# Optimization experiments

Measured on AMD Instinct MI355X. Metric: run time of the kernel, lower is better.

## Reference

```python
import jax, jax.numpy as jnp
import numpy as np

N_EMBD = 1024  # C in forward; scale is C**-0.5 (full embed dim, per source)


def setup_inputs() -> dict:
    key = jax.random.key(0)
    k1, k2, k3, k4 = jax.random.split(key, 4)
    B, T, C, H = 4, 4096, N_EMBD, 64
    x = jax.random.normal(k1, (B, T, C), dtype=jnp.float32)
    # weights stored as [in, out] = [n_embd, head_size]
    Wq = jax.random.normal(k2, (C, H), dtype=jnp.float32) * (C ** -0.5)
    Wk = jax.random.normal(k3, (C, H), dtype=jnp.float32) * (C ** -0.5)
    Wv = jax.random.normal(k4, (C, H), dtype=jnp.float32) * (C ** -0.5)
    return {"x": x, "Wq": Wq, "Wk": Wk, "Wv": Wv}


def reference(x, Wq, Wk, Wv):
    # x: [B, T, C]; projections to head_size H
    C = x.shape[-1]
    q = jnp.einsum('btc,ch->bth', x, Wq)  # [B,T,H]
    k = jnp.einsum('btc,ch->bth', x, Wk)  # [B,T,H]
    v = jnp.einsum('btc,ch->bth', x, Wv)  # [B,T,H]
    # scores scaled by C**-0.5 (full embed dim, matching original module)
    wei = jnp.einsum('bth,bsh->bts', q, k) * (C ** -0.5)  # [B,T,T]
    wei = jax.nn.softmax(wei, axis=-1)  # dropout p=0 -> identity
    out = jnp.einsum('bts,bsh->bth', wei, v)  # [B,T,H]
    return out
```

## Files before the change

### kernel.cpp

```cpp
#include <hip/hip_runtime.h>
#include <hip/hip_bf16.h>


#define BB 4
#define TT 4096
#define CC 1024
#define HH 64

typedef __attribute__((ext_vector_type(8))) short bf16x8;
typedef __attribute__((ext_vector_type(4))) float f32x4;

__device__ __forceinline__ short f2bf(float f) {
  union { float f; unsigned u; } v; v.f = f;
  unsigned r = v.u + 0x7fffu + ((v.u >> 16) & 1u);
  return (short)(r >> 16);
}

__global__ void wtf_kernel(const float* __restrict__ Wq, const float* __restrict__ Wk,
                           const float* __restrict__ Wv, short* __restrict__ WtF) {
  int idx = blockIdx.x * 256 + threadIdx.x;
  int lane = idx & 63, ks = (idx >> 6) & 31, nf = idx >> 11;
  int l15 = lane & 15, lg = lane >> 4;
  int n = nf * 16 + l15;
  const float* W = (n < HH) ? Wq : ((n < 2 * HH) ? Wk : Wv);
  float sc = (n < HH) ? (0.03125f * 1.44269504f) : 1.0f;
  int k0 = ks * 32 + lg * 8, h = n & (HH - 1);
  bf16x8 r;
#pragma unroll
  for (int j = 0; j < 8; ++j) r[j] = f2bf(W[(k0 + j) * HH + h] * sc);
  *(bf16x8*)(WtF + (size_t)idx * 8) = r;
}

__launch_bounds__(256, 4)
__global__ void proj_kernel(const float* __restrict__ x, const short* __restrict__ WtF,
                            short* __restrict__ qo, short* __restrict__ ko,
                            short* __restrict__ vTo) {
  __shared__ __align__(16) short xs[16 * 1024];
  int t = threadIdx.x;
  int row0 = blockIdx.x * 16;

  {
    int r = t >> 4, kc = t & 15;
    const float4* xr4 = (const float4*)(x + (size_t)(row0 + r) * CC) + kc * 2;
#pragma unroll
    for (int i = 0; i < 8; ++i) {
      float4 a = xr4[i * 32], b2 = xr4[i * 32 + 1];
      bf16x8 w;
      w[0] = f2bf(a.x);  w[1] = f2bf(a.y);  w[2] = f2bf(a.z);  w[3] = f2bf(a.w);
      w[4] = f2bf(b2.x); w[5] = f2bf(b2.y); w[6] = f2bf(b2.z); w[7] = f2bf(b2.w);
      int c = kc + i * 16;
      int S = (c * 256 + r * 16) ^ ((c & 7) << 4);
      *(bf16x8*)((char*)xs + S) = w;
    }
  }
  __syncthreads();

  int wave = t >> 6, lane = t & 63;
  int l15 = lane & 15, lg = lane >> 4;
  int nf0 = wave * 3;
  const short* wp = WtF + ((size_t)nf0 * 32 * 64 + (size_t)lane) * 8;
  const char* xsb = (const char*)xs;

  f32x4 acc[3];
#pragma unroll
  for (int j = 0; j < 3; ++j) acc[j] = (f32x4){0.f, 0.f, 0.f, 0.f};

  bf16x8 wA[3], wB[3];
#pragma unroll
  for (int j = 0; j < 3; ++j) wA[j] = *(const bf16x8*)(wp + (size_t)j * 32 * 512);

#pragma unroll
  for (int ks = 0; ks < 32; ks += 2) {
#pragma unroll
    for (int j = 0; j < 3; ++j)
      wB[j] = *(const bf16x8*)(wp + ((size_t)j * 32 + ks + 1) * 512);
    bf16x8 a0 = *(const bf16x8*)(xsb + ks * 1024 +
                   ((lane * 16) ^ ((((ks * 4) + lg) & 7) << 4)));
#pragma unroll
    for (int j = 0; j < 3; ++j)
      acc[j] = __builtin_amdgcn_mfma_f32_16x16x32_bf16(a0, wA[j], acc[j], 0, 0, 0);
    if (ks + 2 < 32) {
#pragma unroll
      for (int j = 0; j < 3; ++j)
        wA[j] = *(const bf16x8*)(wp + ((size_t)j * 32 + ks + 2) * 512);
    }
    bf16x8 a1 = *(const bf16x8*)(xsb + (ks + 1) * 1024 +
                   ((lane * 16) ^ (((((ks + 1) * 4) + lg) & 7) << 4)));
#pragma unroll
    for (int j = 0; j < 3; ++j)
      acc[j] = __builtin_amdgcn_mfma_f32_16x16x32_bf16(a1, wB[j], acc[j], 0, 0, 0);
  }

#pragma unroll
  for (int j = 0; j < 3; ++j) {
    int nf = nf0 + j;
    int h = (nf & 3) * 16 + l15;
    if (nf < 8) {
      short* dst = (nf < 4) ? qo : ko;
#pragma unroll
      for (int reg = 0; reg < 4; ++reg)
        dst[(size_t)(row0 + lg * 4 + reg) * HH + h] = f2bf(acc[j][reg]);
    } else {
      int b = row0 >> 12;
      int trow = (row0 & 4095) + lg * 4;
      short4 s4;
      s4.x = f2bf(acc[j][0]); s4.y = f2bf(acc[j][1]);
      s4.z = f2bf(acc[j][2]); s4.w = f2bf(acc[j][3]);
      *(short4*)(vTo + ((size_t)b * HH + h) * TT + trow) = s4;
    }
  }
}

__global__ void kperm_kernel(const short* __restrict__ k, short* __restrict__ kF) {
  int idx = blockIdx.x * 256 + threadIdx.x;
  int lane = idx & 63, ld = (idx >> 6) & 7, kt = (idx >> 9) & 63, b = idx >> 15;
  int l15 = lane & 15, lg = lane >> 4;
  int kpos = kt * 64 + (ld >> 1) * 16 + l15;
  int e0 = (ld & 1) * 32 + lg * 8;
  bf16x8 r = *(const bf16x8*)(k + ((size_t)b * TT + kpos) * HH + e0);
  *(bf16x8*)(kF + (size_t)idx * 8) = r;
}

__global__ void vperm_kernel(const short* __restrict__ vT, short* __restrict__ vF) {
  int idx = blockIdx.x * 256 + threadIdx.x;
  int lane = idx & 63, ld = (idx >> 6) & 7, kt = (idx >> 9) & 63, b = idx >> 15;
  int l15 = lane & 15, lg = lane >> 4;
  int h = (ld >> 1) * 16 + l15;
  int spos = kt * 64 + (ld & 1) * 32 + lg * 8;
  bf16x8 r = *(const bf16x8*)(vT + ((size_t)b * HH + h) * TT + spos);
  *(bf16x8*)(vF + (size_t)idx * 8) = r;
}

__launch_bounds__(512, 2)
__global__ void attnQ_kernel(const short* __restrict__ q, const short* __restrict__ kF,
                             const short* __restrict__ vF, float* __restrict__ out) {
  __shared__ __align__(16) short ps[8][1280];
  __shared__ __align__(16) float macc[64][68];
  __shared__ float lL[64];
  int wave = threadIdx.x >> 6, lane = threadIdx.x & 63;
  int l15 = lane & 15, lg = lane >> 4;
  int qg = wave & 1, qr = wave >> 1;
  int low3 = blockIdx.x & 7;
  int b  = low3 >> 1;
  int qt = ((blockIdx.x >> 3) << 1) | (low3 & 1);
  int brow0 = qt * 64;
  int rowW = brow0 + qg * 32;

  const short* qb = q + ((size_t)b * TT + rowW + l15) * HH;
  bf16x8 qa[2][2];
  qa[0][0] = *(const bf16x8*)(qb + lg * 8);
  qa[0][1] = *(const bf16x8*)(qb + 32 + lg * 8);
  qa[1][0] = *(const bf16x8*)(qb + 16 * HH + lg * 8);
  qa[1][1] = *(const bf16x8*)(qb + 16 * HH + 32 + lg * 8);

  const short* kfb = kF + (size_t)b * (64 * 8 * 64 * 8) + (size_t)lane * 8;
  const short* vfb = vF + (size_t)b * (64 * 8 * 64 * 8) + (size_t)lane * 8;

  f32x4 acc[2][4];
#pragma unroll
  for (int g = 0; g < 2; ++g)
#pragma unroll
    for (int i = 0; i < 4; ++i) acc[g][i] = (f32x4){0.f, 0.f, 0.f, 0.f};
  float lsum[2][4] = {{0.f, 0.f, 0.f, 0.f}, {0.f, 0.f, 0.f, 0.f}};

  char* psw = (char*)&ps[wave][0];
  int pw = lg * 4 * 80 + ((l15 * 2) ^ ((lg >> 1) << 4));
  int pr = l15 * 80 + ((lg ^ (l15 >> 3)) << 4);

  for (int t = qr * 32; t < qr * 32 + 32; ++t) {
    const short* kp = kfb + (size_t)t * 2048;
    const short* vp = vfb + (size_t)(t >> 1) * 4096 + (size_t)(t & 1) * 512;
    bf16x8 kf[4], vf[4];
#pragma unroll
    for (int ld = 0; ld < 4; ++ld) kf[ld] = *(const bf16x8*)(kp + ld * 512);
#pragma unroll
    for (int hf = 0; hf < 4; ++hf) vf[hf] = *(const bf16x8*)(vp + hf * 1024);
#pragma unroll
    for (int g = 0; g < 2; ++g)
#pragma unroll
      for (int cf = 0; cf < 2; ++cf) {
        f32x4 t4 = (f32x4){0.f, 0.f, 0.f, 0.f};
        t4 = __builtin_amdgcn_mfma_f32_16x16x32_bf16(qa[g][0], kf[cf * 2], t4, 0, 0, 0);
        t4 = __builtin_amdgcn_mfma_f32_16x16x32_bf16(qa[g][1], kf[cf * 2 + 1], t4, 0, 0, 0);
#pragma unroll
        for (int reg = 0; reg < 4; ++reg) {
          float p = exp2f(t4[reg]);
          lsum[g][reg] += p;
          *(short*)(psw + (g * 1280 + pw + reg * 80 + cf * 32)) = f2bf(p);
        }
      }
    bf16x8 pa0 = *(const bf16x8*)(psw + pr);
    bf16x8 pa1 = *(const bf16x8*)(psw + 1280 + pr);
    __builtin_amdgcn_s_setprio(1);
#pragma unroll
    for (int hf = 0; hf < 4; ++hf) {
      acc[0][hf] = __builtin_amdgcn_mfma_f32_16x16x32_bf16(pa0, vf[hf], acc[0][hf], 0, 0, 0);
      acc[1][hf] = __builtin_amdgcn_mfma_f32_16x16x32_bf16(pa1, vf[hf], acc[1][hf], 0, 0, 0);
    }
    __builtin_amdgcn_s_setprio(0);
  }

#pragma unroll
  for (int g = 0; g < 2; ++g)
#pragma unroll
    for (int reg = 0; reg < 4; ++reg) {
      float r = lsum[g][reg];
      r += __shfl_xor(r, 1); r += __shfl_xor(r, 2);
      r += __shfl_xor(r, 4); r += __shfl_xor(r, 8);
      lsum[g][reg] = r;
    }

#pragma unroll
  for (int ph = 0; ph < 4; ++ph) {
    if (qr == ph) {
#pragma unroll
      for (int g = 0; g < 2; ++g) {
#pragma unroll
        for (int reg = 0; reg < 4; ++reg) {
          int row = qg * 32 + g * 16 + lg * 4 + reg;
          if (ph == 0) {
#pragma unroll
            for (int hf = 0; hf < 4; ++hf)
              macc[row][hf * 16 + l15] = acc[g][hf][reg];
            if (l15 == 0) lL[row] = lsum[g][reg];
          } else {
#pragma unroll
            for (int hf = 0; hf < 4; ++hf)
              macc[row][hf * 16 + l15] += acc[g][hf][reg];
            if (l15 == 0) lL[row] += lsum[g][reg];
          }
        }
      }
    }
    __syncthreads();
  }

  {
    int t = threadIdx.x;
    int r = t >> 3, c0 = (t & 7) * 8;
    float linv = 1.0f / lL[r];
    float4 o0, o1;
    o0.x = macc[r][c0 + 0] * linv; o0.y = macc[r][c0 + 1] * linv;
    o0.z = macc[r][c0 + 2] * linv; o0.w = macc[r][c0 + 3] * linv;
    o1.x = macc[r][c0 + 4] * linv; o1.y = macc[r][c0 + 5] * linv;
    o1.z = macc[r][c0 + 6] * linv; o1.w = macc[r][c0 + 7] * linv;
    float* op = out + ((size_t)b * TT + brow0 + r) * HH + c0;
    *(float4*)op = o0;
    *(float4*)(op + 4) = o1;
  }
}

extern "C" void kernel_launch(void* const* d_in, const int* in_sizes, int n_in,
                              void* d_out, int out_size, void* d_ws, size_t ws_size,
                              hipStream_t stream) {
  const float* x  = (const float*)d_in[0];
  const float* Wq = (const float*)d_in[1];
  const float* Wk = (const float*)d_in[2];
  const float* Wv = (const float*)d_in[3];
  float* out = (float*)d_out;

  char* ws = (char*)d_ws;
  short* WtF = (short*)ws;
  short* q   = (short*)(ws + 0x080000);
  short* k   = (short*)(ws + 0x280000);
  short* vT  = (short*)(ws + 0x480000);
  short* kF  = (short*)(ws + 0x680000);
  short* vF  = (short*)(ws + 0x880000);

  hipLaunchKernelGGL(wtf_kernel,   dim3(96),   dim3(256), 0, stream, Wq, Wk, Wv, WtF);
  hipLaunchKernelGGL(proj_kernel,  dim3(1024), dim3(256), 0, stream, x, WtF, q, k, vT);
  hipLaunchKernelGGL(kperm_kernel, dim3(512),  dim3(256), 0, stream, k, kF);
  hipLaunchKernelGGL(vperm_kernel, dim3(512),  dim3(256), 0, stream, vT, vF);
  hipLaunchKernelGGL(attnQ_kernel, dim3(256),  dim3(512), 0, stream, q, kF, vF, out);
}
```

Baseline: 76.28 us.

## Give each attention wave all 64 query rows and double-buffer K/V register loads

The attention kernel now splits the key range across all 8 waves, each wave covering all 64 query rows (4 row groups) instead of 32 rows over 4 key splits. Each loaded K/V fragment is therefore reused across twice as many query rows, which cuts global/L2 traffic per MFMA. The next key tile is prefetched into a second register set while the current one is computed, to hide load latency. Probabilities are converted with the library bf16 conversion. The cost is more registers (larger accumulators plus double buffers), more LDS for P, and an 8-phase reduction of partial results.

```diff
diff --git a/kernel.cpp b/kernel.cpp
--- a/kernel.cpp
+++ b/kernel.cpp
@@ -14,6 +14,11 @@
   union { float f; unsigned u; } v; v.f = f;
   unsigned r = v.u + 0x7fffu + ((v.u >> 16) & 1u);
   return (short)(r >> 16);
+}
+
+__device__ __forceinline__ short f2bf_hw(float f) {
+  __hip_bfloat16 h = __float2bfloat16(f);
+  return *reinterpret_cast<short*>(&h);
 }
 
 __global__ void wtf_kernel(const float* __restrict__ Wq, const float* __restrict__ Wk,
@@ -131,77 +136,101 @@
   *(bf16x8*)(vF + (size_t)idx * 8) = r;
 }
 
-__launch_bounds__(512, 2)
-__global__ void attnQ_kernel(const short* __restrict__ q, const short* __restrict__ kF,
-                             const short* __restrict__ vF, float* __restrict__ out) {
-  __shared__ __align__(16) short ps[8][1280];
+
+#define A64_BODY(KC, VC, KN, VN, T_CUR)                                         \
+  {                                                                             \
+    int tn_ = ((T_CUR) + 1 < ktN) ? (T_CUR) + 1 : kt0;                          \
+    const short* kpn_ = kfb + (size_t)tn_ * 2048;                               \
+    const short* vpn_ = vfb + (size_t)(tn_ >> 1) * 4096 + (size_t)(tn_ & 1) * 512; \
+    _Pragma("unroll")                                                           \
+    for (int ld = 0; ld < 4; ++ld) KN[ld] = *(const bf16x8*)(kpn_ + ld * 512);  \
+    _Pragma("unroll")                                                           \
+    for (int hf = 0; hf < 4; ++hf) VN[hf] = *(const bf16x8*)(vpn_ + hf * 1024); \
+    _Pragma("unroll")                                                           \
+    for (int g = 0; g < 4; ++g) {                                               \
+      _Pragma("unroll")                                                         \
+      for (int cf = 0; cf < 2; ++cf) {                                          \
+        f32x4 t4_ = (f32x4){0.f, 0.f, 0.f, 0.f};                                \
+        t4_ = __builtin_amdgcn_mfma_f32_16x16x32_bf16(qa[g][0], KC[cf * 2], t4_, 0, 0, 0); \
+        t4_ = __builtin_amdgcn_mfma_f32_16x16x32_bf16(qa[g][1], KC[cf * 2 + 1], t4_, 0, 0, 0); \
+        _Pragma("unroll")                                                       \
+        for (int reg = 0; reg < 4; ++reg) {                                     \
+          float p_ = exp2f(t4_[reg]);                                           \
+          lsum[g][reg] += p_;                                                   \
+          *(short*)(psw + (g * 1280 + pw + reg * 80 + cf * 32)) = f2bf_hw(p_);  \
+        }                                                                       \
+      }                                                                         \
+    }                                                                           \
+    __builtin_amdgcn_s_setprio(1);                                              \
+    _Pragma("unroll")                                                           \
+    for (int g = 0; g < 4; ++g) {                                               \
+      bf16x8 pa_ = *(const bf16x8*)(psw + g * 1280 + pr);                       \
+      _Pragma("unroll")                                                         \
+      for (int hf = 0; hf < 4; ++hf)                                            \
+        acc[g][hf] = __builtin_amdgcn_mfma_f32_16x16x32_bf16(pa_, VC[hf], acc[g][hf], 0, 0, 0); \
+    }                                                                           \
+    __builtin_amdgcn_s_setprio(0);                                              \
+  }
+
+__global__ __launch_bounds__(512) __attribute__((amdgpu_waves_per_eu(2, 2)))
+void attn64_kernel(const short* __restrict__ q, const short* __restrict__ kF,
+                   const short* __restrict__ vF, float* __restrict__ out) {
+  __shared__ __align__(16) short ps[8][2560];
   __shared__ __align__(16) float macc[64][68];
   __shared__ float lL[64];
   int wave = threadIdx.x >> 6, lane = threadIdx.x & 63;
   int l15 = lane & 15, lg = lane >> 4;
-  int qg = wave & 1, qr = wave >> 1;
+  int qr = wave;
   int low3 = blockIdx.x & 7;
   int b  = low3 >> 1;
   int qt = ((blockIdx.x >> 3) << 1) | (low3 & 1);
   int brow0 = qt * 64;
-  int rowW = brow0 + qg * 32;
-
-  const short* qb = q + ((size_t)b * TT + rowW + l15) * HH;
-  bf16x8 qa[2][2];
-  qa[0][0] = *(const bf16x8*)(qb + lg * 8);
-  qa[0][1] = *(const bf16x8*)(qb + 32 + lg * 8);
-  qa[1][0] = *(const bf16x8*)(qb + 16 * HH + lg * 8);
-  qa[1][1] = *(const bf16x8*)(qb + 16 * HH + 32 + lg * 8);
+
+  const short* qb = q + ((size_t)b * TT + brow0 + l15) * HH;
+  bf16x8 qa[4][2];
+#pragma unroll
+  for (int g = 0; g < 4; ++g) {
+    qa[g][0] = *(const bf16x8*)(qb + g * 16 * HH + lg * 8);
+    qa[g][1] = *(const bf16x8*)(qb + g * 16 * HH + 32 + lg * 8);
+  }
 
   const short* kfb = kF + (size_t)b * (64 * 8 * 64 * 8) + (size_t)lane * 8;
   const short* vfb = vF + (size_t)b * (64 * 8 * 64 * 8) + (size_t)lane * 8;
 
-  f32x4 acc[2][4];
-#pragma unroll
-  for (int g = 0; g < 2; ++g)
+  f32x4 acc[4][4];
+#pragma unroll
+  for (int g = 0; g < 4; ++g)
 #pragma unroll
     for (int i = 0; i < 4; ++i) acc[g][i] = (f32x4){0.f, 0.f, 0.f, 0.f};
-  float lsum[2][4] = {{0.f, 0.f, 0.f, 0.f}, {0.f, 0.f, 0.f, 0.f}};
+  float lsum[4][4];
+#pragma unroll
+  for (int g = 0; g < 4; ++g)
+#pragma unroll
+    for (int i = 0; i < 4; ++i) lsum[g][i] = 0.f;
 
   char* psw = (char*)&ps[wave][0];
-  int pw = lg * 4 * 80 + ((l15 * 2) ^ ((lg >> 1) << 4));
+  int pw = lg * 320 + ((l15 * 2) ^ ((lg >> 1) << 4));
   int pr = l15 * 80 + ((lg ^ (l15 >> 3)) << 4);
 
-  for (int t = qr * 32; t < qr * 32 + 32; ++t) {
-    const short* kp = kfb + (size_t)t * 2048;
-    const short* vp = vfb + (size_t)(t >> 1) * 4096 + (size_t)(t & 1) * 512;
-    bf16x8 kf[4], vf[4];
-#pragma unroll
-    for (int ld = 0; ld < 4; ++ld) kf[ld] = *(const bf16x8*)(kp + ld * 512);
-#pragma unroll
-    for (int hf = 0; hf < 4; ++hf) vf[hf] = *(const bf16x8*)(vp + hf * 1024);
-#pragma unroll
-    for (int g = 0; g < 2; ++g)
-#pragma unroll
-      for (int cf = 0; cf < 2; ++cf) {
-        f32x4 t4 = (f32x4){0.f, 0.f, 0.f, 0.f};
-        t4 = __builtin_amdgcn_mfma_f32_16x16x32_bf16(qa[g][0], kf[cf * 2], t4, 0, 0, 0);
-        t4 = __builtin_amdgcn_mfma_f32_16x16x32_bf16(qa[g][1], kf[cf * 2 + 1], t4, 0, 0, 0);
-#pragma unroll
-        for (int reg = 0; reg < 4; ++reg) {
-          float p = exp2f(t4[reg]);
-          lsum[g][reg] += p;
-          *(short*)(psw + (g * 1280 + pw + reg * 80 + cf * 32)) = f2bf(p);
-        }
-      }
-    bf16x8 pa0 = *(const bf16x8*)(psw + pr);
-    bf16x8 pa1 = *(const bf16x8*)(psw + 1280 + pr);
-    __builtin_amdgcn_s_setprio(1);
-#pragma unroll
-    for (int hf = 0; hf < 4; ++hf) {
-      acc[0][hf] = __builtin_amdgcn_mfma_f32_16x16x32_bf16(pa0, vf[hf], acc[0][hf], 0, 0, 0);
-      acc[1][hf] = __builtin_amdgcn_mfma_f32_16x16x32_bf16(pa1, vf[hf], acc[1][hf], 0, 0, 0);
-    }
-    __builtin_amdgcn_s_setprio(0);
-  }
-
-#pragma unroll
-  for (int g = 0; g < 2; ++g)
+  int kt0 = qr * 16, ktN = kt0 + 16;
+
+  bf16x8 kcA[4], vcA[4], kcB[4], vcB[4];
+  {
+    const short* kp = kfb + (size_t)kt0 * 2048;
+    const short* vp = vfb + (size_t)(kt0 >> 1) * 4096 + (size_t)(kt0 & 1) * 512;
+#pragma unroll
+    for (int ld = 0; ld < 4; ++ld) kcA[ld] = *(const bf16x8*)(kp + ld * 512);
+#pragma unroll
+    for (int hf = 0; hf < 4; ++hf) vcA[hf] = *(const bf16x8*)(vp + hf * 1024);
+  }
+
+  for (int t = kt0; t < ktN; t += 2) {
+    A64_BODY(kcA, vcA, kcB, vcB, t)
+    A64_BODY(kcB, vcB, kcA, vcA, t + 1)
+  }
+
+#pragma unroll
+  for (int g = 0; g < 4; ++g)
 #pragma unroll
     for (int reg = 0; reg < 4; ++reg) {
       float r = lsum[g][reg];
@@ -211,13 +240,13 @@
     }
 
 #pragma unroll
-  for (int ph = 0; ph < 4; ++ph) {
+  for (int ph = 0; ph < 8; ++ph) {
     if (qr == ph) {
 #pragma unroll
-      for (int g = 0; g < 2; ++g) {
+      for (int g = 0; g < 4; ++g)
 #pragma unroll
         for (int reg = 0; reg < 4; ++reg) {
-          int row = qg * 32 + g * 16 + lg * 4 + reg;
+          int row = g * 16 + lg * 4 + reg;
           if (ph == 0) {
 #pragma unroll
             for (int hf = 0; hf < 4; ++hf)
@@ -230,7 +259,6 @@
             if (l15 == 0) lL[row] += lsum[g][reg];
           }
         }
-      }
     }
     __syncthreads();
   }
@@ -267,9 +295,9 @@
   short* kF  = (short*)(ws + 0x680000);
   short* vF  = (short*)(ws + 0x880000);
 
-  hipLaunchKernelGGL(wtf_kernel,   dim3(96),   dim3(256), 0, stream, Wq, Wk, Wv, WtF);
-  hipLaunchKernelGGL(proj_kernel,  dim3(1024), dim3(256), 0, stream, x, WtF, q, k, vT);
-  hipLaunchKernelGGL(kperm_kernel, dim3(512),  dim3(256), 0, stream, k, kF);
-  hipLaunchKernelGGL(vperm_kernel, dim3(512),  dim3(256), 0, stream, vT, vF);
-  hipLaunchKernelGGL(attnQ_kernel, dim3(256),  dim3(512), 0, stream, q, kF, vF, out);
-}
+  hipLaunchKernelGGL(wtf_kernel,    dim3(96),   dim3(256), 0, stream, Wq, Wk, Wv, WtF);
+  hipLaunchKernelGGL(proj_kernel,   dim3(1024), dim3(256), 0, stream, x, WtF, q, k, vT);
+  hipLaunchKernelGGL(kperm_kernel,  dim3(512),  dim3(256), 0, stream, k, kF);
+  hipLaunchKernelGGL(vperm_kernel,  dim3(512),  dim3(256), 0, stream, vT, vF);
+  hipLaunchKernelGGL(attn64_kernel, dim3(256),  dim3(512), 0, stream, q, kF, vF, out);
+}
```

Measured after the change: 81.31 us. 6.6% more time.

## Stage K/V tiles through LDS with triple-buffered async global-to-LDS loads

Applied to the files above, without the earlier changes.

The attention kernel now has all eight waves cooperatively stream K and V tiles into a three-slot LDS ring using global_load_lds, with vmcnt waits and barriers, so loads for step t+2 overlap compute on step t. Before, each wave loaded its own K/V fragments directly from global memory at the point of use. Each tile is now fetched once per block and shared, which cuts redundant global traffic and hides load latency. In exchange it uses about 96KB more LDS and adds a block-wide barrier every iteration. The bf16 conversion also switches to the library intrinsic.

```diff
diff --git a/kernel.cpp b/kernel.cpp
--- a/kernel.cpp
+++ b/kernel.cpp
@@ -15,6 +15,19 @@
   unsigned r = v.u + 0x7fffu + ((v.u >> 16) & 1u);
   return (short)(r >> 16);
 }
+
+__device__ __forceinline__ short f2bf_hw(float f) {
+  __hip_bfloat16 h = __float2bfloat16(f);
+  return *reinterpret_cast<short*>(&h);
+}
+
+__device__ __forceinline__ void gload16(const short* g, short* l) {
+  __builtin_amdgcn_global_load_lds(
+      (const __attribute__((address_space(1))) void*)g,
+      (__attribute__((address_space(3))) void*)l, 16, 0, 0);
+}
+
+#define WAITVM(N) asm volatile("s_waitcnt vmcnt(" #N ")" ::: "memory")
 
 __global__ void wtf_kernel(const float* __restrict__ Wq, const float* __restrict__ Wk,
                            const float* __restrict__ Wv, short* __restrict__ WtF) {
@@ -131,30 +144,84 @@
   *(bf16x8*)(vF + (size_t)idx * 8) = r;
 }
 
-__launch_bounds__(512, 2)
-__global__ void attnQ_kernel(const short* __restrict__ q, const short* __restrict__ kF,
-                             const short* __restrict__ vF, float* __restrict__ out) {
+
+#define STAGE(T)                                                                \
+  {                                                                             \
+    const short* src_ = gsb + (size_t)(2 * (T) + ktl_s) * 4096;                 \
+    short* dst_ = ldsSb + ((T) % 3) * 16384;                                    \
+    _Pragma("unroll")                                                           \
+    for (int i = 0; i < 4; ++i) gload16(src_ + i * 512, dst_ + i * 512);        \
+  }
+
+#define COMPUTE(T)                                                              \
+  {                                                                             \
+    const short* bufB_ = kvs + ((T) % 3) * 16384;                               \
+    const short* ldsK_ = bufB_ + ktl_c * 4096 + halfk_c * 2048;                 \
+    const short* ldsV_ = bufB_ + 8192 + ktl_c * 4096 + halfk_c * 512;           \
+    bf16x8 kf_[4], vf_[4];                                                      \
+    _Pragma("unroll")                                                           \
+    for (int j = 0; j < 4; ++j)                                                 \
+      kf_[j] = *(const bf16x8*)(ldsK_ + j * 512 + lane * 8);                    \
+    _Pragma("unroll")                                                           \
+    for (int hf = 0; hf < 4; ++hf)                                              \
+      vf_[hf] = *(const bf16x8*)(ldsV_ + hf * 1024 + lane * 8);                 \
+    _Pragma("unroll")                                                           \
+    for (int g = 0; g < 2; ++g) {                                               \
+      _Pragma("unroll")                                                         \
+      for (int cf = 0; cf < 2; ++cf) {                                          \
+        f32x4 t4_ = (f32x4){0.f, 0.f, 0.f, 0.f};                                \
+        t4_ = __builtin_amdgcn_mfma_f32_16x16x32_bf16(qa[g][0], kf_[cf * 2], t4_, 0, 0, 0); \
+        t4_ = __builtin_amdgcn_mfma_f32_16x16x32_bf16(qa[g][1], kf_[cf * 2 + 1], t4_, 0, 0, 0); \
+        _Pragma("unroll")                                                       \
+        for (int reg = 0; reg < 4; ++reg) {                                     \
+          float p_ = exp2f(t4_[reg]);                                           \
+          lsum[g][reg] += p_;                                                   \
+          *(short*)(psw + (g * 1280 + pw + reg * 80 + cf * 32)) = f2bf_hw(p_);  \
+        }                                                                       \
+      }                                                                         \
+    }                                                                           \
+    bf16x8 pa0_ = *(const bf16x8*)(psw + pr);                                   \
+    bf16x8 pa1_ = *(const bf16x8*)(psw + 1280 + pr);                            \
+    __builtin_amdgcn_s_setprio(1);                                              \
+    _Pragma("unroll")                                                           \
+    for (int hf = 0; hf < 4; ++hf) {                                            \
+      acc[0][hf] = __builtin_amdgcn_mfma_f32_16x16x32_bf16(pa0_, vf_[hf], acc[0][hf], 0, 0, 0); \
+      acc[1][hf] = __builtin_amdgcn_mfma_f32_16x16x32_bf16(pa1_, vf_[hf], acc[1][hf], 0, 0, 0); \
+    }                                                                           \
+    __builtin_amdgcn_s_setprio(0);                                              \
+  }
+
+__global__ __launch_bounds__(512) __attribute__((amdgpu_waves_per_eu(2, 2)))
+void attnP_kernel(const short* __restrict__ q, const short* __restrict__ kF,
+                  const short* __restrict__ vF, float* __restrict__ out) {
+  __shared__ __align__(16) short kvs[3 * 16384];
   __shared__ __align__(16) short ps[8][1280];
   __shared__ __align__(16) float macc[64][68];
   __shared__ float lL[64];
   int wave = threadIdx.x >> 6, lane = threadIdx.x & 63;
   int l15 = lane & 15, lg = lane >> 4;
   int qg = wave & 1, qr = wave >> 1;
+  int ktl_c = qr >> 1, halfk_c = qr & 1;
   int low3 = blockIdx.x & 7;
   int b  = low3 >> 1;
   int qt = ((blockIdx.x >> 3) << 1) | (low3 & 1);
   int brow0 = qt * 64;
-  int rowW = brow0 + qg * 32;
-
-  const short* qb = q + ((size_t)b * TT + rowW + l15) * HH;
+
+  const short* qb = q + ((size_t)b * TT + brow0 + qg * 32 + l15) * HH;
   bf16x8 qa[2][2];
-  qa[0][0] = *(const bf16x8*)(qb + lg * 8);
-  qa[0][1] = *(const bf16x8*)(qb + 32 + lg * 8);
-  qa[1][0] = *(const bf16x8*)(qb + 16 * HH + lg * 8);
-  qa[1][1] = *(const bf16x8*)(qb + 16 * HH + 32 + lg * 8);
-
-  const short* kfb = kF + (size_t)b * (64 * 8 * 64 * 8) + (size_t)lane * 8;
-  const short* vfb = vF + (size_t)b * (64 * 8 * 64 * 8) + (size_t)lane * 8;
+#pragma unroll
+  for (int g = 0; g < 2; ++g) {
+    qa[g][0] = *(const bf16x8*)(qb + g * 16 * HH + lg * 8);
+    qa[g][1] = *(const bf16x8*)(qb + g * 16 * HH + 32 + lg * 8);
+  }
+
+  const short* kfb = kF + (size_t)b * 262144;
+  const short* vfb = vF + (size_t)b * 262144;
+
+  int sec = wave >> 1;
+  int isV_s = sec >> 1, ktl_s = sec & 1, cb = (wave & 1) * 4;
+  const short* gsb = (isV_s ? vfb : kfb) + cb * 512 + lane * 8;
+  short* ldsSb = kvs + sec * 4096 + cb * 512;
 
   f32x4 acc[2][4];
 #pragma unroll
@@ -164,41 +231,20 @@
   float lsum[2][4] = {{0.f, 0.f, 0.f, 0.f}, {0.f, 0.f, 0.f, 0.f}};
 
   char* psw = (char*)&ps[wave][0];
-  int pw = lg * 4 * 80 + ((l15 * 2) ^ ((lg >> 1) << 4));
+  int pw = lg * 320 + ((l15 * 2) ^ ((lg >> 1) << 4));
   int pr = l15 * 80 + ((lg ^ (l15 >> 3)) << 4);
 
-  for (int t = qr * 32; t < qr * 32 + 32; ++t) {
-    const short* kp = kfb + (size_t)t * 2048;
-    const short* vp = vfb + (size_t)(t >> 1) * 4096 + (size_t)(t & 1) * 512;
-    bf16x8 kf[4], vf[4];
-#pragma unroll
-    for (int ld = 0; ld < 4; ++ld) kf[ld] = *(const bf16x8*)(kp + ld * 512);
-#pragma unroll
-    for (int hf = 0; hf < 4; ++hf) vf[hf] = *(const bf16x8*)(vp + hf * 1024);
-#pragma unroll
-    for (int g = 0; g < 2; ++g)
-#pragma unroll
-      for (int cf = 0; cf < 2; ++cf) {
-        f32x4 t4 = (f32x4){0.f, 0.f, 0.f, 0.f};
-        t4 = __builtin_amdgcn_mfma_f32_16x16x32_bf16(qa[g][0], kf[cf * 2], t4, 0, 0, 0);
-        t4 = __builtin_amdgcn_mfma_f32_16x16x32_bf16(qa[g][1], kf[cf * 2 + 1], t4, 0, 0, 0);
-#pragma unroll
-        for (int reg = 0; reg < 4; ++reg) {
-          float p = exp2f(t4[reg]);
-          lsum[g][reg] += p;
-          *(short*)(psw + (g * 1280 + pw + reg * 80 + cf * 32)) = f2bf(p);
-        }
-      }
-    bf16x8 pa0 = *(const bf16x8*)(psw + pr);
-    bf16x8 pa1 = *(const bf16x8*)(psw + 1280 + pr);
-    __builtin_amdgcn_s_setprio(1);
-#pragma unroll
-    for (int hf = 0; hf < 4; ++hf) {
-      acc[0][hf] = __builtin_amdgcn_mfma_f32_16x16x32_bf16(pa0, vf[hf], acc[0][hf], 0, 0, 0);
-      acc[1][hf] = __builtin_amdgcn_mfma_f32_16x16x32_bf16(pa1, vf[hf], acc[1][hf], 0, 0, 0);
-    }
-    __builtin_amdgcn_s_setprio(0);
-  }
+  STAGE(0)
+  STAGE(1)
+
+  for (int t = 0; t < 30; ++t) {
+    WAITVM(4);
+    __builtin_amdgcn_s_barrier();
+    STAGE(t + 2)
+    COMPUTE(t)
+  }
+  WAITVM(4);  __builtin_amdgcn_s_barrier();  COMPUTE(30)
+  WAITVM(0);  __builtin_amdgcn_s_barrier();  COMPUTE(31)
 
 #pragma unroll
   for (int g = 0; g < 2; ++g)
@@ -214,7 +260,7 @@
   for (int ph = 0; ph < 4; ++ph) {
     if (qr == ph) {
 #pragma unroll
-      for (int g = 0; g < 2; ++g) {
+      for (int g = 0; g < 2; ++g)
 #pragma unroll
         for (int reg = 0; reg < 4; ++reg) {
           int row = qg * 32 + g * 16 + lg * 4 + reg;
@@ -230,14 +276,13 @@
             if (l15 == 0) lL[row] += lsum[g][reg];
           }
         }
-      }
     }
     __syncthreads();
   }
 
   {
-    int t = threadIdx.x;
-    int r = t >> 3, c0 = (t & 7) * 8;
+    int tt = threadIdx.x;
+    int r = tt >> 3, c0 = (tt & 7) * 8;
     float linv = 1.0f / lL[r];
     float4 o0, o1;
     o0.x = macc[r][c0 + 0] * linv; o0.y = macc[r][c0 + 1] * linv;
@@ -271,5 +316,5 @@
   hipLaunchKernelGGL(proj_kernel,  dim3(1024), dim3(256), 0, stream, x, WtF, q, k, vT);
   hipLaunchKernelGGL(kperm_kernel, dim3(512),  dim3(256), 0, stream, k, kF);
   hipLaunchKernelGGL(vperm_kernel, dim3(512),  dim3(256), 0, stream, vT, vF);
-  hipLaunchKernelGGL(attnQ_kernel, dim3(256),  dim3(512), 0, stream, q, kF, vF, out);
-}
+  hipLaunchKernelGGL(attnP_kernel, dim3(256),  dim3(512), 0, stream, q, kF, vF, out);
+}
```

Result: slower. 90.87 us (+19.1%).

## Split attention into 32-row blocks with 8-way key split and MFMA row sums

Applied to the files above, without the earlier changes.

The attention kernel now gives each block 32 query rows instead of 64 and splits the 4096 keys eight ways across waves, doubling the grid to 512 blocks and raising occupancy bounds. Row sums of P are computed by an extra MFMA against a ones vector instead of scalar adds and shuffle reductions. exp2 uses the hardware builtin and bf16 rounding is simplified. This aims to fill more CUs and cut VALU work, at the cost of more K/V rereads per query row and a longer serialized LDS merge across eight waves.

```diff
diff --git a/kernel.cpp b/kernel.cpp
--- a/kernel.cpp
+++ b/kernel.cpp
@@ -10,10 +10,21 @@
 typedef __attribute__((ext_vector_type(8))) short bf16x8;
 typedef __attribute__((ext_vector_type(4))) float f32x4;
 
+#if __has_builtin(__builtin_amdgcn_exp2f)
+#define EXP2(x) __builtin_amdgcn_exp2f(x)
+#else
+#define EXP2(x) exp2f(x)
+#endif
+
 __device__ __forceinline__ short f2bf(float f) {
   union { float f; unsigned u; } v; v.f = f;
   unsigned r = v.u + 0x7fffu + ((v.u >> 16) & 1u);
   return (short)(r >> 16);
+}
+
+__device__ __forceinline__ short p2bf(float f) {
+  union { float f; unsigned u; } v; v.f = f;
+  return (short)((v.u + 0x8000u) >> 16);
 }
 
 __global__ void wtf_kernel(const float* __restrict__ Wq, const float* __restrict__ Wk,
@@ -131,43 +142,47 @@
   *(bf16x8*)(vF + (size_t)idx * 8) = r;
 }
 
-__launch_bounds__(512, 2)
-__global__ void attnQ_kernel(const short* __restrict__ q, const short* __restrict__ kF,
+__launch_bounds__(512, 4)
+__global__ void attnW_kernel(const short* __restrict__ q, const short* __restrict__ kF,
                              const short* __restrict__ vF, float* __restrict__ out) {
-  __shared__ __align__(16) short ps[8][1280];
-  __shared__ __align__(16) float macc[64][68];
-  __shared__ float lL[64];
+  __shared__ __align__(16) short ps[8][2560];
+  __shared__ __align__(16) float macc[32][68];
+  __shared__ float lL[32];
   int wave = threadIdx.x >> 6, lane = threadIdx.x & 63;
   int l15 = lane & 15, lg = lane >> 4;
-  int qg = wave & 1, qr = wave >> 1;
   int low3 = blockIdx.x & 7;
   int b  = low3 >> 1;
   int qt = ((blockIdx.x >> 3) << 1) | (low3 & 1);
-  int brow0 = qt * 64;
-  int rowW = brow0 + qg * 32;
-
-  const short* qb = q + ((size_t)b * TT + rowW + l15) * HH;
+  int brow0 = qt * 32;
+
+  const short* qb = q + ((size_t)b * TT + brow0 + l15) * HH;
   bf16x8 qa[2][2];
-  qa[0][0] = *(const bf16x8*)(qb + lg * 8);
-  qa[0][1] = *(const bf16x8*)(qb + 32 + lg * 8);
-  qa[1][0] = *(const bf16x8*)(qb + 16 * HH + lg * 8);
-  qa[1][1] = *(const bf16x8*)(qb + 16 * HH + 32 + lg * 8);
-
-  const short* kfb = kF + (size_t)b * (64 * 8 * 64 * 8) + (size_t)lane * 8;
-  const short* vfb = vF + (size_t)b * (64 * 8 * 64 * 8) + (size_t)lane * 8;
-
-  f32x4 acc[2][4];
-#pragma unroll
-  for (int g = 0; g < 2; ++g)
+#pragma unroll
+  for (int g = 0; g < 2; ++g) {
+    qa[g][0] = *(const bf16x8*)(qb + g * 16 * HH + lg * 8);
+    qa[g][1] = *(const bf16x8*)(qb + g * 16 * HH + 32 + lg * 8);
+  }
+
+  bf16x8 ones;
+#pragma unroll
+  for (int j = 0; j < 8; ++j) ones[j] = (short)0x3F80;
+
+  const short* kfb = kF + (size_t)b * 262144 + (size_t)lane * 8;
+  const short* vfb = vF + (size_t)b * 262144 + (size_t)lane * 8;
+
+  f32x4 acc[2][4], accl[2];
+#pragma unroll
+  for (int g = 0; g < 2; ++g) {
 #pragma unroll
     for (int i = 0; i < 4; ++i) acc[g][i] = (f32x4){0.f, 0.f, 0.f, 0.f};
-  float lsum[2][4] = {{0.f, 0.f, 0.f, 0.f}, {0.f, 0.f, 0.f, 0.f}};
+    accl[g] = (f32x4){0.f, 0.f, 0.f, 0.f};
+  }
 
   char* psw = (char*)&ps[wave][0];
-  int pw = lg * 4 * 80 + ((l15 * 2) ^ ((lg >> 1) << 4));
+  int pw = lg * 320 + ((l15 * 2) ^ ((lg >> 1) << 4));
   int pr = l15 * 80 + ((lg ^ (l15 >> 3)) << 4);
 
-  for (int t = qr * 32; t < qr * 32 + 32; ++t) {
+  for (int t = wave * 16; t < wave * 16 + 16; ++t) {
     const short* kp = kfb + (size_t)t * 2048;
     const short* vp = vfb + (size_t)(t >> 1) * 4096 + (size_t)(t & 1) * 512;
     bf16x8 kf[4], vf[4];
@@ -184,9 +199,8 @@
         t4 = __builtin_amdgcn_mfma_f32_16x16x32_bf16(qa[g][1], kf[cf * 2 + 1], t4, 0, 0, 0);
 #pragma unroll
         for (int reg = 0; reg < 4; ++reg) {
-          float p = exp2f(t4[reg]);
-          lsum[g][reg] += p;
-          *(short*)(psw + (g * 1280 + pw + reg * 80 + cf * 32)) = f2bf(p);
+          float p = EXP2(t4[reg]);
+          *(short*)(psw + (g * 1280 + pw + reg * 80 + cf * 32)) = p2bf(p);
         }
       }
     bf16x8 pa0 = *(const bf16x8*)(psw + pr);
@@ -197,56 +211,43 @@
       acc[0][hf] = __builtin_amdgcn_mfma_f32_16x16x32_bf16(pa0, vf[hf], acc[0][hf], 0, 0, 0);
       acc[1][hf] = __builtin_amdgcn_mfma_f32_16x16x32_bf16(pa1, vf[hf], acc[1][hf], 0, 0, 0);
     }
+    accl[0] = __builtin_amdgcn_mfma_f32_16x16x32_bf16(pa0, ones, accl[0], 0, 0, 0);
+    accl[1] = __builtin_amdgcn_mfma_f32_16x16x32_bf16(pa1, ones, accl[1], 0, 0, 0);
     __builtin_amdgcn_s_setprio(0);
   }
 
 #pragma unroll
-  for (int g = 0; g < 2; ++g)
-#pragma unroll
-    for (int reg = 0; reg < 4; ++reg) {
-      float r = lsum[g][reg];
-      r += __shfl_xor(r, 1); r += __shfl_xor(r, 2);
-      r += __shfl_xor(r, 4); r += __shfl_xor(r, 8);
-      lsum[g][reg] = r;
-    }
-
-#pragma unroll
-  for (int ph = 0; ph < 4; ++ph) {
-    if (qr == ph) {
-#pragma unroll
-      for (int g = 0; g < 2; ++g) {
+  for (int ph = 0; ph < 8; ++ph) {
+    if (wave == ph) {
+#pragma unroll
+      for (int g = 0; g < 2; ++g)
 #pragma unroll
         for (int reg = 0; reg < 4; ++reg) {
-          int row = qg * 32 + g * 16 + lg * 4 + reg;
+          int row = g * 16 + lg * 4 + reg;
           if (ph == 0) {
 #pragma unroll
             for (int hf = 0; hf < 4; ++hf)
               macc[row][hf * 16 + l15] = acc[g][hf][reg];
-            if (l15 == 0) lL[row] = lsum[g][reg];
+            if (l15 == 0) lL[row] = accl[g][reg];
           } else {
 #pragma unroll
             for (int hf = 0; hf < 4; ++hf)
               macc[row][hf * 16 + l15] += acc[g][hf][reg];
-            if (l15 == 0) lL[row] += lsum[g][reg];
+            if (l15 == 0) lL[row] += accl[g][reg];
           }
         }
-      }
     }
     __syncthreads();
   }
 
   {
-    int t = threadIdx.x;
-    int r = t >> 3, c0 = (t & 7) * 8;
+    int tt = threadIdx.x;
+    int r = tt >> 4, c0 = (tt & 15) * 4;
     float linv = 1.0f / lL[r];
-    float4 o0, o1;
-    o0.x = macc[r][c0 + 0] * linv; o0.y = macc[r][c0 + 1] * linv;
-    o0.z = macc[r][c0 + 2] * linv; o0.w = macc[r][c0 + 3] * linv;
-    o1.x = macc[r][c0 + 4] * linv; o1.y = macc[r][c0 + 5] * linv;
-    o1.z = macc[r][c0 + 6] * linv; o1.w = macc[r][c0 + 7] * linv;
-    float* op = out + ((size_t)b * TT + brow0 + r) * HH + c0;
-    *(float4*)op = o0;
-    *(float4*)(op + 4) = o1;
+    float4 o;
+    o.x = macc[r][c0 + 0] * linv; o.y = macc[r][c0 + 1] * linv;
+    o.z = macc[r][c0 + 2] * linv; o.w = macc[r][c0 + 3] * linv;
+    *(float4*)(out + ((size_t)b * TT + brow0 + r) * HH + c0) = o;
   }
 }
 
@@ -271,5 +272,5 @@
   hipLaunchKernelGGL(proj_kernel,  dim3(1024), dim3(256), 0, stream, x, WtF, q, k, vT);
   hipLaunchKernelGGL(kperm_kernel, dim3(512),  dim3(256), 0, stream, k, kF);
   hipLaunchKernelGGL(vperm_kernel, dim3(512),  dim3(256), 0, stream, vT, vF);
-  hipLaunchKernelGGL(attnQ_kernel, dim3(256),  dim3(512), 0, stream, q, kF, vF, out);
-}
+  hipLaunchKernelGGL(attnW_kernel, dim3(512),  dim3(512), 0, stream, q, kF, vF, out);
+}
```

Measured after the change: 69.29 us. 1.1x faster.
